# Optimization experiments

Measured on AMD Instinct MI355X. Metric: run time of the kernel, lower is better.

## Reference

```python
import jax, jax.numpy as jnp
import numpy as np

B, S, D = 8, 1024, 1024
H, DH = 16, 64  # num_attention_heads, attention_head_size; H*DH == D


def setup_inputs() -> dict:
    key = jax.random.key(0)
    ks = jax.random.split(key, 6)
    scale = 0.02
    return {
        "hidden_states": jax.random.normal(ks[0], (B, S, D), jnp.float32),
        "right_hidden_states": jax.random.normal(ks[1], (B, S, D), jnp.float32),
        "attention_mask": jnp.ones((B, S, S), jnp.float32),
        "Wq": jax.random.normal(ks[2], (D, H * DH), jnp.float32) * scale,
        "bq": jnp.zeros((H * DH,), jnp.float32),
        "Wk": jax.random.normal(ks[3], (D, H * DH), jnp.float32) * scale,
        "bk": jnp.zeros((H * DH,), jnp.float32),
        "Wv": jax.random.normal(ks[4], (D, H * DH), jnp.float32) * scale,
        "bv": jnp.zeros((H * DH,), jnp.float32),
    }


def _split_heads(x, b):
    # (B, S, H*DH) -> (B, H, S, DH)
    return x.reshape(b, -1, H, DH).transpose(0, 2, 1, 3)


def reference(hidden_states, right_hidden_states, attention_mask, Wq, bq, Wk, bk, Wv, bv):
    b = hidden_states.shape[0]
    q = _split_heads(hidden_states @ Wq + bq, b)          # (B,H,Sq,DH)
    k = _split_heads(right_hidden_states @ Wk + bk, b)    # (B,H,Sk,DH)
    v = _split_heads(right_hidden_states @ Wv + bv, b)    # (B,H,Sk,DH)

    scores = jnp.einsum("bhqd,bhkd->bhqk", q, k) / jnp.sqrt(jnp.asarray(DH, q.dtype))
    scores = jnp.sum(scores, axis=1, keepdims=True)       # (B,1,Sq,Sk) head-summed

    ext = (1.0 - attention_mask[:, None, :, :].astype(scores.dtype)) * -1e9
    probs = jax.nn.softmax(scores + ext, axis=-1)         # (B,1,Sq,Sk)

    ctx = jnp.matmul(probs, v)                            # broadcast -> (B,H,Sq,DH)
    # Faithful to original: reshape WITHOUT transposing heads back.
    return ctx.reshape(b, -1, H * DH)                     # (B,Sq,H*DH)
```

## Files before the change

kernel.cpp:

```cpp
#include <hip/hip_runtime.h>
#include <stdint.h>

constexpr int S = 1024;
constexpr int D = 1024;
constexpr int NB = 8;

typedef __bf16 bf16x8 __attribute__((ext_vector_type(8)));
typedef float floatx4 __attribute__((ext_vector_type(4)));

#define AS1 __attribute__((address_space(1)))
#define AS3 __attribute__((address_space(3)))

__device__ __forceinline__ unsigned short f2bf(float f) {
  unsigned u = __builtin_bit_cast(unsigned, f);
  u += 0x7fffu + ((u >> 16) & 1u);
  return (unsigned short)(u >> 16);
}

__device__ __forceinline__ ushort4 f2bf4(float4 w) {
  ushort4 o;
  o.x = f2bf(w.x); o.y = f2bf(w.y); o.z = f2bf(w.z); o.w = f2bf(w.w);
  return o;
}

__device__ __forceinline__ float bf2f(unsigned short x) {
  unsigned u = ((unsigned)x) << 16;
  return __builtin_bit_cast(float, u);
}

__device__ __forceinline__ void gload16(const void* g, void* l) {
  __builtin_amdgcn_global_load_lds((const AS1 unsigned int*)g, (AS3 unsigned int*)l, 16, 0, 0);
}

__global__ __launch_bounds__(256) void prep_kernel(
    const float4* __restrict__ hs4, const float4* __restrict__ rhs4,
    ushort4* __restrict__ hsb4, ushort4* __restrict__ rhsb4,
    const float* __restrict__ Wq, const float* __restrict__ Wk, const float* __restrict__ Wv,
    unsigned short* __restrict__ WvT, ushort4* __restrict__ Wqb4, ushort4* __restrict__ Wkb4,
    const float* __restrict__ bq, const float* __restrict__ bk, float* __restrict__ u,
    float* __restrict__ v, float* __restrict__ cbuf) {
  __shared__ float tile[32][33];
  __shared__ float bsh[1024];
  __shared__ float sh[256];
  __shared__ int nz2;
  const int bid = blockIdx.x;
  const int tid = threadIdx.x;
  if (bid < 2048) {
    const int base = bid * 256 + tid;
    float4 a0 = hs4[base];
    float4 a1 = hs4[base + 524288];
    float4 a2 = hs4[base + 1048576];
    float4 a3 = hs4[base + 1572864];
    float4 b0 = rhs4[base];
    float4 b1 = rhs4[base + 524288];
    float4 b2 = rhs4[base + 1048576];
    float4 b3 = rhs4[base + 1572864];
    hsb4[base] = f2bf4(a0);
    hsb4[base + 524288] = f2bf4(a1);
    hsb4[base + 1048576] = f2bf4(a2);
    hsb4[base + 1572864] = f2bf4(a3);
    rhsb4[base] = f2bf4(b0);
    rhsb4[base + 524288] = f2bf4(b1);
    rhsb4[base + 1048576] = f2bf4(b2);
    rhsb4[base + 1572864] = f2bf4(b3);
  } else if (bid < 2304) {
    const int base = (bid - 2048) * 256 + tid;
    const float4* Wq4 = (const float4*)Wq;
    const float4* Wk4 = (const float4*)Wk;
    float4 a0 = Wq4[base];
    float4 a1 = Wq4[base + 65536];
    float4 a2 = Wq4[base + 131072];
    float4 a3 = Wq4[base + 196608];
    float4 b0 = Wk4[base];
    float4 b1 = Wk4[base + 65536];
    float4 b2 = Wk4[base + 131072];
    float4 b3 = Wk4[base + 196608];
    Wqb4[base] = f2bf4(a0);
    Wqb4[base + 65536] = f2bf4(a1);
    Wqb4[base + 131072] = f2bf4(a2);
    Wqb4[base + 196608] = f2bf4(a3);
    Wkb4[base] = f2bf4(b0);
    Wkb4[base + 65536] = f2bf4(b1);
    Wkb4[base + 131072] = f2bf4(b2);
    Wkb4[base + 196608] = f2bf4(b3);
  } else if (bid < 3328) {
    const int r = bid - 2304;
    const int bx = (r & 31) * 32;
    const int by = (r >> 5) * 32;
    const int x = tid & 31;
    const int y0 = tid >> 5;
    for (int i = 0; i < 4; ++i) {
      int y = y0 + i * 8;
      tile[y][x] = Wv[(by + y) * D + bx + x];
    }
    __syncthreads();
    for (int i = 0; i < 4; ++i) {
      int y = y0 + i * 8;
      WvT[(long long)(bx + y) * D + by + x] = f2bf(tile[x][y]);
    }
  } else if (bid < 3336) {
    const bool isU = bid < 3332;
    const int blk = isU ? (bid - 3328) : (bid - 3332);
    const float* W = isU ? Wq : Wk;
    const float* bvec = isU ? bk : bq;
    float* outv = isU ? u : v;
    if (tid == 0) nz2 = 0;
    __syncthreads();
    float4 q = ((const float4*)bvec)[tid];
    bsh[tid * 4 + 0] = q.x;
    bsh[tid * 4 + 1] = q.y;
    bsh[tid * 4 + 2] = q.z;
    bsh[tid * 4 + 3] = q.w;
    if (q.x != 0.f || q.y != 0.f || q.z != 0.f || q.w != 0.f) nz2 = 1;
    __syncthreads();
    const int row0 = blk * 256;
    if (!nz2) {
      outv[row0 + tid] = 0.f;
      return;
    }
    const int lane = tid & 63;
    const int wv = tid >> 6;
    for (int rr = 0; rr < 64; ++rr) {
      const int row = row0 + wv * 64 + rr;
      const float* rp = W + (long long)row * 1024;
      float s = 0.f;
#pragma unroll
      for (int k = 0; k < 16; ++k) s += rp[lane + 64 * k] * bsh[lane + 64 * k];
      s += __shfl_xor(s, 32, 64);
      s += __shfl_xor(s, 16, 64);
      s += __shfl_xor(s, 8, 64);
      s += __shfl_xor(s, 4, 64);
      s += __shfl_xor(s, 2, 64);
      s += __shfl_xor(s, 1, 64);
      if (lane == 0) outv[row] = 0.125f * s;
    }
  } else {
    float s = 0.f;
    for (int c = tid; c < 1024; c += 256) s += bq[c] * bk[c];
    sh[tid] = s;
    __syncthreads();
    for (int o = 128; o; o >>= 1) {
      if (tid < o) sh[tid] += sh[tid + o];
      __syncthreads();
    }
    if (tid == 0) cbuf[0] = 0.125f * sh[0];
  }
}


#define GEMM_COMMON_IDX                  \
  const int tid = threadIdx.x;           \
  const int lane = tid & 63;             \
  const int w = tid >> 6;                \
  const int r15 = lane & 15;             \
  const int quad = lane >> 4;            \
  const int pq = (quad ^ ((r15 >> 1) & 3)) * 8; \
  const int wm = (w >> 1) * 64;          \
  const int wn = (w & 1) * 64;

#define GEMM_ACC_INIT                    \
  floatx4 acc[4][4];                     \
  for (int i = 0; i < 4; ++i)            \
    for (int j = 0; j < 4; ++j) acc[i][j] = {0.f, 0.f, 0.f, 0.f};

#define GEMM_STAGE_SETUP32(Abase, lda_, Bbase, ldb_)                          \
  const int srow = tid >> 2;                                                  \
  const int scg = (((tid & 3) ^ ((srow >> 1) & 3)) * 8);                      \
  const unsigned short* aG0 = (Abase) + (long long)srow * (lda_) + scg;       \
  const unsigned short* aG1 = aG0 + (long long)64 * (lda_);                   \
  const unsigned short* bG0 = (Bbase) + (long long)srow * (ldb_) + scg;       \
  const unsigned short* bG1 = bG0 + (long long)64 * (ldb_);                   \
  unsigned short* aL0 = As + w * 512;                                         \
  unsigned short* aL1 = As + w * 512 + 2048;                                  \
  unsigned short* bL0 = Bs + w * 512;                                         \
  unsigned short* bL1 = Bs + w * 512 + 2048;

#define GEMM_KLOOP32(Klen)                                                             \
  for (int k0 = 0; k0 < (Klen); k0 += 32) {                                            \
    gload16(aG0 + k0, aL0);                                                            \
    gload16(aG1 + k0, aL1);                                                            \
    gload16(bG0 + k0, bL0);                                                            \
    gload16(bG1 + k0, bL1);                                                            \
    __syncthreads();                                                                   \
    bf16x8 af[4], bfr[4];                                                              \
    for (int t = 0; t < 4; ++t) {                                                      \
      af[t] = *reinterpret_cast<const bf16x8*>(As + (wm + t * 16 + r15) * 32 + pq);    \
      bfr[t] = *reinterpret_cast<const bf16x8*>(Bs + (wn + t * 16 + r15) * 32 + pq);   \
    }                                                                                  \
    for (int mt = 0; mt < 4; ++mt)                                                     \
      for (int nt = 0; nt < 4; ++nt)                                                   \
        acc[mt][nt] =                                                                  \
            __builtin_amdgcn_mfma_f32_16x16x32_bf16(af[mt], bfr[nt], acc[mt][nt], 0, 0, 0); \
    __syncthreads();                                                                   \
  }

#define GEMM_STAGE_SETUP64(Abase, lda_, Bbase, ldb_)                          \
  const int srow = tid >> 2;                                                  \
  const int scg = (((tid & 3) ^ ((srow >> 1) & 3)) * 8);                      \
  const unsigned short* aG0 = (Abase) + (long long)srow * (lda_) + scg;       \
  const unsigned short* aG1 = aG0 + (long long)64 * (lda_);                   \
  const unsigned short* bG0 = (Bbase) + (long long)srow * (ldb_) + scg;       \
  const unsigned short* bG1 = bG0 + (long long)64 * (ldb_);

#define GEMM_KLOOP64(Klen)                                                               \
  for (int k0 = 0; k0 < (Klen); k0 += 64) {                                              \
    gload16(aG0 + k0, As[0] + w * 512);                                                  \
    gload16(aG1 + k0, As[0] + w * 512 + 2048);                                           \
    gload16(aG0 + k0 + 32, As[1] + w * 512);                                             \
    gload16(aG1 + k0 + 32, As[1] + w * 512 + 2048);                                      \
    gload16(bG0 + k0, Bs[0] + w * 512);                                                  \
    gload16(bG1 + k0, Bs[0] + w * 512 + 2048);                                           \
    gload16(bG0 + k0 + 32, Bs[1] + w * 512);                                             \
    gload16(bG1 + k0 + 32, Bs[1] + w * 512 + 2048);                                      \
    __syncthreads();                                                                     \
    for (int h = 0; h < 2; ++h) {                                                        \
      bf16x8 af[4], bfr[4];                                                              \
      for (int t = 0; t < 4; ++t) {                                                      \
        af[t] = *reinterpret_cast<const bf16x8*>(As[h] + (wm + t * 16 + r15) * 32 + pq); \
        bfr[t] = *reinterpret_cast<const bf16x8*>(Bs[h] + (wn + t * 16 + r15) * 32 + pq);\
      }                                                                                  \
      for (int mt = 0; mt < 4; ++mt)                                                     \
        for (int nt = 0; nt < 4; ++nt)                                                   \
          acc[mt][nt] =                                                                  \
              __builtin_amdgcn_mfma_f32_16x16x32_bf16(af[mt], bfr[nt], acc[mt][nt], 0, 0, 0); \
    }                                                                                    \
    __syncthreads();                                                                     \
  }

__global__ __launch_bounds__(256) void wprod_kernel(
    const unsigned short* __restrict__ Wkb, const unsigned short* __restrict__ Wqb,
    float* __restrict__ Mtf, const unsigned short* __restrict__ hsb,
    const unsigned short* __restrict__ rhsb, const float* __restrict__ u,
    const float* __restrict__ v, const float* __restrict__ cbuf, float* __restrict__ t2,
    float* __restrict__ t3) {
  __shared__ __align__(16) unsigned short As[128 * 32];
  __shared__ __align__(16) unsigned short Bs[128 * 32];
  const int bid = blockIdx.x;
  if (bid < 256) {
    GEMM_COMMON_IDX
    const int tilei = bid & 63;
    const int kc = bid >> 6;
    const int bx = tilei & 7;
    const int by = tilei >> 3;
    const unsigned short* A = Wkb + (long long)by * 128 * D + kc * 256;
    const unsigned short* Bt = Wqb + (long long)bx * 128 * D + kc * 256;
    GEMM_STAGE_SETUP32(A, D, Bt, D)
    GEMM_ACC_INIT
    GEMM_KLOOP32(256)
    float* dst = Mtf + ((long long)kc << 20);
    for (int mt = 0; mt < 4; ++mt)
      for (int nt = 0; nt < 4; ++nt) {
        const int mrow = by * 128 + wm + mt * 16 + quad * 4;
        const int nc = bx * 128 + wn + nt * 16 + r15;
        floatx4 vv = acc[mt][nt];
        for (int e = 0; e < 4; ++e) dst[(long long)(mrow + e) * 1024 + nc] = vv[e] * 0.125f;
      }
  } else {
    const int tid = threadIdx.x;
    const bool isT2 = bid < 288;
    const int row = (isT2 ? (bid - 256) : (bid - 288)) * 256 + tid;
    const float* vec = isT2 ? u : v;
    const unsigned short* mat = isT2 ? hsb : rhsb;
    float* out = isT2 ? t2 : t3;
    __shared__ int nz;
    if (tid == 0) nz = 0;
    __syncthreads();
    const float4* u4 = (const float4*)vec;
    float4 uu = u4[tid];
    if (uu.x != 0.f || uu.y != 0.f || uu.z != 0.f || uu.w != 0.f) nz = 1;
    __syncthreads();
    const float c2 = 0.5f * cbuf[0];
    if (!nz) {
      out[row] = c2;
      return;
    }
    const ushort4* r4 = (const ushort4*)(mat + (long long)row * 1024);
    float s = 0.f;
    for (int c4 = 0; c4 < 256; ++c4) {
      ushort4 h = r4[c4];
      s += bf2f(h.x) * vec[c4 * 4 + 0] + bf2f(h.y) * vec[c4 * 4 + 1] +
           bf2f(h.z) * vec[c4 * 4 + 2] + bf2f(h.w) * vec[c4 * 4 + 3];
    }
    out[row] = s + c2;
  }
}

__global__ __launch_bounds__(256) void castM_kernel(const float4* __restrict__ Mtf4,
                                                    ushort4* __restrict__ Mtb4) {
  const int j = blockIdx.x * 256 + threadIdx.x;
  float4 a = Mtf4[j];
  float4 b = Mtf4[j + 262144];
  float4 c = Mtf4[j + 524288];
  float4 d = Mtf4[j + 786432];
  ushort4 o;
  o.x = f2bf(a.x + b.x + c.x + d.x);
  o.y = f2bf(a.y + b.y + c.y + d.y);
  o.z = f2bf(a.z + b.z + c.z + d.z);
  o.w = f2bf(a.w + b.w + c.w + d.w);
  Mtb4[j] = o;
}

__global__ __launch_bounds__(256) void gemm_fused_kernel(
    const unsigned short* __restrict__ hsb, const unsigned short* __restrict__ rhsb,
    const unsigned short* __restrict__ Mtb, const unsigned short* __restrict__ WvT,
    const float* __restrict__ bv, unsigned short* __restrict__ hsMb,
    unsigned short* __restrict__ Vmt) {
  __shared__ __align__(16) unsigned short As[2][4096];
  __shared__ __align__(16) unsigned short Bs[2][4096];
  GEMM_COMMON_IDX
  const int bid = blockIdx.x;
  const int swz = (bid & 7) * 128 + (bid >> 3);
  const int bx = swz & 15;
  const int by = swz >> 4;
  const int seg = bx >> 3;
  const long long nloc = (long long)(bx & 7) * 128;
  const long long m0 = (long long)by * 128;
  const unsigned short* A = ((seg == 0) ? hsb : rhsb) + m0 * D;
  const unsigned short* Bt = ((seg == 0) ? Mtb : WvT) + nloc * D;

  GEMM_STAGE_SETUP64(A, D, Bt, D)
  GEMM_ACC_INIT
  GEMM_KLOOP64(D)

  for (int mt = 0; mt < 4; ++mt) {
    for (int nt = 0; nt < 4; ++nt) {
      const long long mrow = m0 + wm + mt * 16 + quad * 4;
      const long long nc = nloc + wn + nt * 16 + r15;
      floatx4 vv = acc[mt][nt];
      if (seg == 0) {
        for (int e = 0; e < 4; ++e) hsMb[(mrow + e) * D + nc] = f2bf(vv[e]);
      } else {
        const float bval = bv[nc];
        for (int e = 0; e < 4; ++e) {
          long long m = mrow + e;
          Vmt[(m >> 10) * (long long)(S * D) + nc * S + (m & 1023)] = f2bf(vv[e] + bval);
        }
      }
    }
  }
}

__global__ __launch_bounds__(256) void gemm_scores_kernel(
    const unsigned short* __restrict__ hsMb, const unsigned short* __restrict__ rhsb,
    const float* __restrict__ mask, unsigned short* __restrict__ E, float* __restrict__ rowsumP,
    const float* __restrict__ t2, const float* __restrict__ t3) {
  __shared__ __align__(16) unsigned short As[2][4096];
  __shared__ __align__(16) unsigned short Bs[2][4096];
  GEMM_COMMON_IDX
  const int bid = blockIdx.x;
  const int z = bid & 7;
  const int r = bid >> 3;
  const int by = r >> 3;
  const int bx = r & 7;
  const long long m0 = (long long)by * 128;
  const long long n0 = (long long)bx * 128;
  const unsigned short* A = hsMb + (long long)z * S * D + m0 * D;
  const unsigned short* Bt = rhsb + (long long)z * S * D + n0 * D;

  GEMM_STAGE_SETUP64(A, D, Bt, D)
  GEMM_ACC_INIT
  GEMM_KLOOP64(D)

  const long long zE = (long long)z * S * 1024;
  float rowpart[4][4];
  for (int mt = 0; mt < 4; ++mt)
    for (int e = 0; e < 4; ++e) rowpart[mt][e] = 0.f;

  for (int mt = 0; mt < 4; ++mt) {
    for (int nt = 0; nt < 4; ++nt) {
      const long long mrow = m0 + wm + mt * 16 + quad * 4;
      const long long nc = n0 + wn + nt * 16 + r15;
      const float t3v = t3[z * 1024 + nc];
      floatx4 vv = acc[mt][nt];
      for (int e = 0; e < 4; ++e) {
        long long m = mrow + e;
        float mval = mask[zE + m * 1024 + nc];
        float sc = vv[e] + t2[z * 1024 + m] + t3v + (1.0f - mval) * -1e9f;
        float Ev = __expf(sc);
        E[zE + m * 1024 + nc] = f2bf(Ev);
        rowpart[mt][e] += Ev;
      }
    }
  }
  const int slot = (bx << 11) + ((wn >> 6) << 10);
  for (int mt = 0; mt < 4; ++mt) {
    for (int e = 0; e < 4; ++e) {
      float s = rowpart[mt][e];
      s += __shfl_xor(s, 1, 64);
      s += __shfl_xor(s, 2, 64);
      s += __shfl_xor(s, 4, 64);
      s += __shfl_xor(s, 8, 64);
      if (r15 == 0) {
        int mloc = (int)(m0 + wm + mt * 16 + quad * 4 + e);
        rowsumP[(z << 14) + slot + mloc] = s;
      }
    }
  }
}

__global__ __launch_bounds__(256) void gemm_ctx_kernel(const unsigned short* __restrict__ E,
                                                       const unsigned short* __restrict__ Vmt,
                                                       const float* __restrict__ rowsumP,
                                                       float* __restrict__ out) {
  __shared__ __align__(16) unsigned short As[2][4096];
  __shared__ __align__(16) unsigned short Bs[2][4096];
  __shared__ float rsinv[128];
  GEMM_COMMON_IDX
  const int bid = blockIdx.x;
  const int z = bid & 7;
  const int r = bid >> 3;
  const int by = r >> 3;
  const int bx = r & 7;
  const long long m0 = (long long)by * 128;
  const long long n0 = (long long)bx * 128;
  const unsigned short* A = E + (long long)z * S * 1024 + m0 * 1024;
  const unsigned short* Bt = Vmt + (long long)z * S * D + n0 * D;

  if (tid < 128) {
    float s = 0.f;
    for (int t = 0; t < 16; ++t) s += rowsumP[(z << 14) + (t << 10) + (int)m0 + tid];
    rsinv[tid] = 1.0f / s;
  }

  GEMM_STAGE_SETUP64(A, 1024, Bt, D)
  GEMM_ACC_INIT
  GEMM_KLOOP64(1024)

  for (int mt = 0; mt < 4; ++mt) {
    for (int nt = 0; nt < 4; ++nt) {
      const int r0 = wm + mt * 16 + quad * 4;
      const long long ncol = n0 + wn + nt * 16 + r15;
      floatx4 vv = acc[mt][nt];
      for (int e = 0; e < 4; ++e) {
        long long m = m0 + r0 + e;
        float val = vv[e] * rsinv[r0 + e];
        out[(long long)z * S * D + (ncol >> 6) * (long long)(S * 64) + m * 64 + (ncol & 63)] =
            val;
      }
    }
  }
}

extern "C" void kernel_launch(void* const* d_in, const int* in_sizes, int n_in, void* d_out,
                              int out_size, void* d_ws, size_t ws_size, hipStream_t stream) {
  const float* hs = (const float*)d_in[0];
  const float* rhs = (const float*)d_in[1];
  const float* mask = (const float*)d_in[2];
  const float* Wq = (const float*)d_in[3];
  const float* bq = (const float*)d_in[4];
  const float* Wk = (const float*)d_in[5];
  const float* bk = (const float*)d_in[6];
  const float* Wv = (const float*)d_in[7];
  const float* bv = (const float*)d_in[8];
  float* out = (float*)d_out;
  char* ws = (char*)d_ws;
  const size_t MB = 1ull << 20;
  unsigned short* WvT = (unsigned short*)(ws + 0 * MB);
  unsigned short* Wqb = (unsigned short*)(ws + 2 * MB);
  unsigned short* Wkb = (unsigned short*)(ws + 4 * MB);
  unsigned short* Mtb = (unsigned short*)(ws + 6 * MB);
  float* u = (float*)(ws + 8 * MB);
  float* v = (float*)(ws + 8 * MB + 4096);
  float* cbuf = (float*)(ws + 8 * MB + 8192);
  float* t2 = (float*)(ws + 8 * MB + 16384);
  float* t3 = (float*)(ws + 8 * MB + 49152);
  float* rowsumP = (float*)(ws + 8 * MB + 131072);
  unsigned short* hsb = (unsigned short*)(ws + 9 * MB);
  unsigned short* rhsb = (unsigned short*)(ws + 25 * MB);
  unsigned short* hsMb = (unsigned short*)(ws + 41 * MB);
  float* Mtf = (float*)(ws + 41 * MB);
  unsigned short* Vmt = (unsigned short*)(ws + 57 * MB);
  unsigned short* E = (unsigned short*)(ws + 9 * MB);

  prep_kernel<<<3337, 256, 0, stream>>>((const float4*)hs, (const float4*)rhs, (ushort4*)hsb,
                                        (ushort4*)rhsb, Wq, Wk, Wv, WvT, (ushort4*)Wqb,
                                        (ushort4*)Wkb, bq, bk, u, v, cbuf);

  wprod_kernel<<<320, 256, 0, stream>>>(Wkb, Wqb, Mtf, hsb, rhsb, u, v, cbuf, t2, t3);
  castM_kernel<<<1024, 256, 0, stream>>>((const float4*)Mtf, (ushort4*)Mtb);

  gemm_fused_kernel<<<1024, 256, 0, stream>>>(hsb, rhsb, Mtb, WvT, bv, hsMb, Vmt);

  gemm_scores_kernel<<<512, 256, 0, stream>>>(hsMb, rhsb, mask, E, rowsumP, t2, t3);

  gemm_ctx_kernel<<<512, 256, 0, stream>>>(E, Vmt, rowsumP, out);
}
```

Measured before the change: 263.2 us.

## Fold weight-product GEMM into prep kernel and merge bias-term pass into fused GEMM

The Wk·Wqᵀ product is now computed directly inside prep_kernel as 256 blocks of 64x64 tiles. Each block converts the fp32 weights to bf16 on the fly, so the separate weight-cast, split-K fp32 partial writes and castM reduction are gone. The t2/t3 bias dot products move into extra blocks of gemm_fused_kernel, reading the fp32 inputs directly. This removes two launches and large fp32 intermediate traffic. The cost is a non-pipelined, full-K per-block GEMM that may leave a long tail in prep_kernel.

```diff
diff --git a/kernel.cpp b/kernel.cpp
--- a/kernel.cpp
+++ b/kernel.cpp
@@ -23,11 +23,6 @@
   return o;
 }
 
-__device__ __forceinline__ float bf2f(unsigned short x) {
-  unsigned u = ((unsigned)x) << 16;
-  return __builtin_bit_cast(float, u);
-}
-
 __device__ __forceinline__ void gload16(const void* g, void* l) {
   __builtin_amdgcn_global_load_lds((const AS1 unsigned int*)g, (AS3 unsigned int*)l, 16, 0, 0);
 }
@@ -36,17 +31,67 @@
     const float4* __restrict__ hs4, const float4* __restrict__ rhs4,
     ushort4* __restrict__ hsb4, ushort4* __restrict__ rhsb4,
     const float* __restrict__ Wq, const float* __restrict__ Wk, const float* __restrict__ Wv,
-    unsigned short* __restrict__ WvT, ushort4* __restrict__ Wqb4, ushort4* __restrict__ Wkb4,
+    unsigned short* __restrict__ WvT, unsigned short* __restrict__ Mtb,
     const float* __restrict__ bq, const float* __restrict__ bk, float* __restrict__ u,
     float* __restrict__ v, float* __restrict__ cbuf) {
   __shared__ float tile[32][33];
   __shared__ float bsh[1024];
   __shared__ float sh[256];
   __shared__ int nz2;
+  __shared__ __align__(16) unsigned short Am[64 * 32];
+  __shared__ __align__(16) unsigned short Bm[64 * 32];
   const int bid = blockIdx.x;
   const int tid = threadIdx.x;
-  if (bid < 2048) {
-    const int base = bid * 256 + tid;
+  if (bid < 256) {
+    const int bx = bid & 15;
+    const int by = bid >> 4;
+    const int srow = tid >> 2;
+    const int scg8 = (((tid & 3) ^ ((srow >> 1) & 3)) * 8);
+    const int lw8 = (tid & 3) * 8;
+    const float* aGp = Wk + (long long)(by * 64 + srow) * 1024 + scg8;
+    const float* bGp = Wq + (long long)(bx * 64 + srow) * 1024 + scg8;
+    const int lane = tid & 63;
+    const int w4 = tid >> 6;
+    const int r15 = lane & 15;
+    const int quad = lane >> 4;
+    const int pq = (quad ^ ((r15 >> 1) & 3)) * 8;
+    const int wm2 = (w4 >> 1) * 32;
+    const int wn2 = (w4 & 1) * 32;
+    floatx4 acc[2][2];
+    for (int i = 0; i < 2; ++i)
+      for (int j = 0; j < 2; ++j) acc[i][j] = {0.f, 0.f, 0.f, 0.f};
+    for (int k0 = 0; k0 < 1024; k0 += 32) {
+      float4 a0 = *(const float4*)(aGp + k0);
+      float4 a1 = *(const float4*)(aGp + k0 + 4);
+      float4 b0 = *(const float4*)(bGp + k0);
+      float4 b1 = *(const float4*)(bGp + k0 + 4);
+      ushort4 ua0 = f2bf4(a0), ua1 = f2bf4(a1), ub0 = f2bf4(b0), ub1 = f2bf4(b1);
+      __syncthreads();
+      *(ushort4*)(Am + srow * 32 + lw8) = ua0;
+      *(ushort4*)(Am + srow * 32 + lw8 + 4) = ua1;
+      *(ushort4*)(Bm + srow * 32 + lw8) = ub0;
+      *(ushort4*)(Bm + srow * 32 + lw8 + 4) = ub1;
+      __syncthreads();
+      bf16x8 af[2], bfr[2];
+      for (int t = 0; t < 2; ++t) {
+        af[t] = *reinterpret_cast<const bf16x8*>(Am + (wm2 + t * 16 + r15) * 32 + pq);
+        bfr[t] = *reinterpret_cast<const bf16x8*>(Bm + (wn2 + t * 16 + r15) * 32 + pq);
+      }
+      for (int mt = 0; mt < 2; ++mt)
+        for (int nt = 0; nt < 2; ++nt)
+          acc[mt][nt] =
+              __builtin_amdgcn_mfma_f32_16x16x32_bf16(af[mt], bfr[nt], acc[mt][nt], 0, 0, 0);
+    }
+    for (int mt = 0; mt < 2; ++mt)
+      for (int nt = 0; nt < 2; ++nt) {
+        const int mr = by * 64 + wm2 + mt * 16 + quad * 4;
+        const int nc = bx * 64 + wn2 + nt * 16 + r15;
+        floatx4 vv = acc[mt][nt];
+        for (int e = 0; e < 4; ++e)
+          Mtb[(long long)(mr + e) * 1024 + nc] = f2bf(vv[e] * 0.125f);
+      }
+  } else if (bid < 2304) {
+    const int base = (bid - 256) * 256 + tid;
     float4 a0 = hs4[base];
     float4 a1 = hs4[base + 524288];
     float4 a2 = hs4[base + 1048576];
@@ -63,26 +108,6 @@
     rhsb4[base + 524288] = f2bf4(b1);
     rhsb4[base + 1048576] = f2bf4(b2);
     rhsb4[base + 1572864] = f2bf4(b3);
-  } else if (bid < 2304) {
-    const int base = (bid - 2048) * 256 + tid;
-    const float4* Wq4 = (const float4*)Wq;
-    const float4* Wk4 = (const float4*)Wk;
-    float4 a0 = Wq4[base];
-    float4 a1 = Wq4[base + 65536];
-    float4 a2 = Wq4[base + 131072];
-    float4 a3 = Wq4[base + 196608];
-    float4 b0 = Wk4[base];
-    float4 b1 = Wk4[base + 65536];
-    float4 b2 = Wk4[base + 131072];
-    float4 b3 = Wk4[base + 196608];
-    Wqb4[base] = f2bf4(a0);
-    Wqb4[base + 65536] = f2bf4(a1);
-    Wqb4[base + 131072] = f2bf4(a2);
-    Wqb4[base + 196608] = f2bf4(a3);
-    Wkb4[base] = f2bf4(b0);
-    Wkb4[base + 65536] = f2bf4(b1);
-    Wkb4[base + 131072] = f2bf4(b2);
-    Wkb4[base + 196608] = f2bf4(b3);
   } else if (bid < 3328) {
     const int r = bid - 2304;
     const int bx = (r & 31) * 32;
@@ -162,37 +187,6 @@
   floatx4 acc[4][4];                     \
   for (int i = 0; i < 4; ++i)            \
     for (int j = 0; j < 4; ++j) acc[i][j] = {0.f, 0.f, 0.f, 0.f};
-
-#define GEMM_STAGE_SETUP32(Abase, lda_, Bbase, ldb_)                          \
-  const int srow = tid >> 2;                                                  \
-  const int scg = (((tid & 3) ^ ((srow >> 1) & 3)) * 8);                      \
-  const unsigned short* aG0 = (Abase) + (long long)srow * (lda_) + scg;       \
-  const unsigned short* aG1 = aG0 + (long long)64 * (lda_);                   \
-  const unsigned short* bG0 = (Bbase) + (long long)srow * (ldb_) + scg;       \
-  const unsigned short* bG1 = bG0 + (long long)64 * (ldb_);                   \
-  unsigned short* aL0 = As + w * 512;                                         \
-  unsigned short* aL1 = As + w * 512 + 2048;                                  \
-  unsigned short* bL0 = Bs + w * 512;                                         \
-  unsigned short* bL1 = Bs + w * 512 + 2048;
-
-#define GEMM_KLOOP32(Klen)                                                             \
-  for (int k0 = 0; k0 < (Klen); k0 += 32) {                                            \
-    gload16(aG0 + k0, aL0);                                                            \
-    gload16(aG1 + k0, aL1);                                                            \
-    gload16(bG0 + k0, bL0);                                                            \
-    gload16(bG1 + k0, bL1);                                                            \
-    __syncthreads();                                                                   \
-    bf16x8 af[4], bfr[4];                                                              \
-    for (int t = 0; t < 4; ++t) {                                                      \
-      af[t] = *reinterpret_cast<const bf16x8*>(As + (wm + t * 16 + r15) * 32 + pq);    \
-      bfr[t] = *reinterpret_cast<const bf16x8*>(Bs + (wn + t * 16 + r15) * 32 + pq);   \
-    }                                                                                  \
-    for (int mt = 0; mt < 4; ++mt)                                                     \
-      for (int nt = 0; nt < 4; ++nt)                                                   \
-        acc[mt][nt] =                                                                  \
-            __builtin_amdgcn_mfma_f32_16x16x32_bf16(af[mt], bfr[nt], acc[mt][nt], 0, 0, 0); \
-    __syncthreads();                                                                   \
-  }
 
 #define GEMM_STAGE_SETUP64(Abase, lda_, Bbase, ldb_)                          \
   const int srow = tid >> 2;                                                  \
@@ -227,88 +221,44 @@
     __syncthreads();                                                                     \
   }
 
-__global__ __launch_bounds__(256) void wprod_kernel(
-    const unsigned short* __restrict__ Wkb, const unsigned short* __restrict__ Wqb,
-    float* __restrict__ Mtf, const unsigned short* __restrict__ hsb,
-    const unsigned short* __restrict__ rhsb, const float* __restrict__ u,
-    const float* __restrict__ v, const float* __restrict__ cbuf, float* __restrict__ t2,
-    float* __restrict__ t3) {
-  __shared__ __align__(16) unsigned short As[128 * 32];
-  __shared__ __align__(16) unsigned short Bs[128 * 32];
-  const int bid = blockIdx.x;
-  if (bid < 256) {
-    GEMM_COMMON_IDX
-    const int tilei = bid & 63;
-    const int kc = bid >> 6;
-    const int bx = tilei & 7;
-    const int by = tilei >> 3;
-    const unsigned short* A = Wkb + (long long)by * 128 * D + kc * 256;
-    const unsigned short* Bt = Wqb + (long long)bx * 128 * D + kc * 256;
-    GEMM_STAGE_SETUP32(A, D, Bt, D)
-    GEMM_ACC_INIT
-    GEMM_KLOOP32(256)
-    float* dst = Mtf + ((long long)kc << 20);
-    for (int mt = 0; mt < 4; ++mt)
-      for (int nt = 0; nt < 4; ++nt) {
-        const int mrow = by * 128 + wm + mt * 16 + quad * 4;
-        const int nc = bx * 128 + wn + nt * 16 + r15;
-        floatx4 vv = acc[mt][nt];
-        for (int e = 0; e < 4; ++e) dst[(long long)(mrow + e) * 1024 + nc] = vv[e] * 0.125f;
-      }
-  } else {
-    const int tid = threadIdx.x;
-    const bool isT2 = bid < 288;
-    const int row = (isT2 ? (bid - 256) : (bid - 288)) * 256 + tid;
-    const float* vec = isT2 ? u : v;
-    const unsigned short* mat = isT2 ? hsb : rhsb;
-    float* out = isT2 ? t2 : t3;
-    __shared__ int nz;
-    if (tid == 0) nz = 0;
-    __syncthreads();
-    const float4* u4 = (const float4*)vec;
-    float4 uu = u4[tid];
-    if (uu.x != 0.f || uu.y != 0.f || uu.z != 0.f || uu.w != 0.f) nz = 1;
-    __syncthreads();
-    const float c2 = 0.5f * cbuf[0];
-    if (!nz) {
-      out[row] = c2;
-      return;
-    }
-    const ushort4* r4 = (const ushort4*)(mat + (long long)row * 1024);
-    float s = 0.f;
-    for (int c4 = 0; c4 < 256; ++c4) {
-      ushort4 h = r4[c4];
-      s += bf2f(h.x) * vec[c4 * 4 + 0] + bf2f(h.y) * vec[c4 * 4 + 1] +
-           bf2f(h.z) * vec[c4 * 4 + 2] + bf2f(h.w) * vec[c4 * 4 + 3];
-    }
-    out[row] = s + c2;
-  }
-}
-
-__global__ __launch_bounds__(256) void castM_kernel(const float4* __restrict__ Mtf4,
-                                                    ushort4* __restrict__ Mtb4) {
-  const int j = blockIdx.x * 256 + threadIdx.x;
-  float4 a = Mtf4[j];
-  float4 b = Mtf4[j + 262144];
-  float4 c = Mtf4[j + 524288];
-  float4 d = Mtf4[j + 786432];
-  ushort4 o;
-  o.x = f2bf(a.x + b.x + c.x + d.x);
-  o.y = f2bf(a.y + b.y + c.y + d.y);
-  o.z = f2bf(a.z + b.z + c.z + d.z);
-  o.w = f2bf(a.w + b.w + c.w + d.w);
-  Mtb4[j] = o;
-}
-
 __global__ __launch_bounds__(256) void gemm_fused_kernel(
     const unsigned short* __restrict__ hsb, const unsigned short* __restrict__ rhsb,
     const unsigned short* __restrict__ Mtb, const unsigned short* __restrict__ WvT,
     const float* __restrict__ bv, unsigned short* __restrict__ hsMb,
-    unsigned short* __restrict__ Vmt) {
+    unsigned short* __restrict__ Vmt, const float* __restrict__ hs,
+    const float* __restrict__ rhs, const float* __restrict__ u, const float* __restrict__ v,
+    const float* __restrict__ cbuf, float* __restrict__ t2, float* __restrict__ t3) {
   __shared__ __align__(16) unsigned short As[2][4096];
   __shared__ __align__(16) unsigned short Bs[2][4096];
   GEMM_COMMON_IDX
   const int bid = blockIdx.x;
+  if (bid >= 1024) {
+    __shared__ int nz;
+    const bool isT2 = bid < 1056;
+    const int row = ((isT2 ? bid - 1024 : bid - 1056) << 8) + tid;
+    const float* vec = isT2 ? u : v;
+    const float* mat = isT2 ? hs : rhs;
+    float* outp = isT2 ? t2 : t3;
+    if (tid == 0) nz = 0;
+    __syncthreads();
+    float4 q = ((const float4*)vec)[tid];
+    if (q.x != 0.f || q.y != 0.f || q.z != 0.f || q.w != 0.f) nz = 1;
+    __syncthreads();
+    const float c2 = 0.5f * cbuf[0];
+    if (!nz) {
+      outp[row] = c2;
+      return;
+    }
+    const float4* r4 = (const float4*)(mat + (long long)row * 1024);
+    float s = 0.f;
+    for (int c4 = 0; c4 < 256; ++c4) {
+      float4 h = r4[c4];
+      s += h.x * vec[c4 * 4 + 0] + h.y * vec[c4 * 4 + 1] + h.z * vec[c4 * 4 + 2] +
+           h.w * vec[c4 * 4 + 3];
+    }
+    outp[row] = s + c2;
+    return;
+  }
   const int swz = (bid & 7) * 128 + (bid >> 3);
   const int bx = swz & 15;
   const int by = swz >> 4;
@@ -456,9 +406,7 @@
   char* ws = (char*)d_ws;
   const size_t MB = 1ull << 20;
   unsigned short* WvT = (unsigned short*)(ws + 0 * MB);
-  unsigned short* Wqb = (unsigned short*)(ws + 2 * MB);
-  unsigned short* Wkb = (unsigned short*)(ws + 4 * MB);
-  unsigned short* Mtb = (unsigned short*)(ws + 6 * MB);
+  unsigned short* Mtb = (unsigned short*)(ws + 2 * MB);
   float* u = (float*)(ws + 8 * MB);
   float* v = (float*)(ws + 8 * MB + 4096);
   float* cbuf = (float*)(ws + 8 * MB + 8192);
@@ -468,18 +416,15 @@
   unsigned short* hsb = (unsigned short*)(ws + 9 * MB);
   unsigned short* rhsb = (unsigned short*)(ws + 25 * MB);
   unsigned short* hsMb = (unsigned short*)(ws + 41 * MB);
-  float* Mtf = (float*)(ws + 41 * MB);
   unsigned short* Vmt = (unsigned short*)(ws + 57 * MB);
   unsigned short* E = (unsigned short*)(ws + 9 * MB);
 
   prep_kernel<<<3337, 256, 0, stream>>>((const float4*)hs, (const float4*)rhs, (ushort4*)hsb,
-                                        (ushort4*)rhsb, Wq, Wk, Wv, WvT, (ushort4*)Wqb,
-                                        (ushort4*)Wkb, bq, bk, u, v, cbuf);
-
-  wprod_kernel<<<320, 256, 0, stream>>>(Wkb, Wqb, Mtf, hsb, rhsb, u, v, cbuf, t2, t3);
-  castM_kernel<<<1024, 256, 0, stream>>>((const float4*)Mtf, (ushort4*)Mtb);
-
-  gemm_fused_kernel<<<1024, 256, 0, stream>>>(hsb, rhsb, Mtb, WvT, bv, hsMb, Vmt);
+                                        (ushort4*)rhsb, Wq, Wk, Wv, WvT, Mtb, bq, bk, u, v,
+                                        cbuf);
+
+  gemm_fused_kernel<<<1088, 256, 0, stream>>>(hsb, rhsb, Mtb, WvT, bv, hsMb, Vmt, hs, rhs, u,
+                                              v, cbuf, t2, t3);
 
   gemm_scores_kernel<<<512, 256, 0, stream>>>(hsMb, rhsb, mask, E, rowsumP, t2, t3);
 
```

Result: no change. 267.1 us (+1.5%).
